# Optimization experiments

Hardware: AMD Instinct MI355X
Metric: run time of the kernel (lower is better)

Reference implementation:

```python
import jax, jax.numpy as jnp
from jax import lax
import numpy as np

N_X, N_Y, N_OBS = 30, 50, 256
ITERS, LR = 400, 0.05


def project_simplex(v):
    # Euclidean projection of a 1-D vector onto the probability simplex.
    n = v.shape[0]
    u = jnp.sort(v)[::-1]
    css = jnp.cumsum(u) - 1.0
    idx = jnp.arange(1, n + 1, dtype=v.dtype)
    rho = jnp.sum((u - css / idx) > 0)
    tau = jnp.take(css, rho - 1) / rho.astype(v.dtype)
    return jnp.maximum(v - tau, 0.0)


def worst_case(r, delta):
    # Exact value of the Ben-Tal et al. total-variation DRO inner problem:
    #   min_{eta, lam>=0} eta + delta*lam + mean_i max(-lam, r_i - eta)
    #   s.t. r_i - eta <= lam
    # = sup_{p in simplex, ||p - 1/N||_1 <= delta} p @ r
    # Closed form: move mass a = min(delta/2, (N-1)/N) from the smallest
    # entries (each holds 1/N nominal mass) onto the largest entry.
    n = r.shape[0]
    nf = jnp.asarray(n, r.dtype)
    a = jnp.minimum(delta * 0.5, (nf - 1.0) / nf)
    s = jnp.sort(r)  # ascending
    w = jnp.clip(a - jnp.arange(n, dtype=r.dtype) / nf, 0.0, 1.0 / nf)
    return jnp.mean(r) + a * jnp.max(r) - jnp.sum(w * s)


def _forward(X, Y, W, b, delta, gamma):
    Y_hat = X @ W.T + b                      # (n_obs, n_y) predictions
    ep = Y - Y_hat                           # (n_obs, n_y) residuals, shared

    def solve_one(y_hat_t):
        # Convex DRO problem per scenario, prisk = p_var: (ep_i @ z - c)^2.
        # Eliminating (eta, lam, obj_aux) analytically via worst_case(), the
        # problem reduces to min over z in simplex, c in R of
        #   worst_case((ep @ z - c)^2, delta) - gamma * (y_hat_t @ z)
        # solved with projected gradient descent (unrolled, fixed iters).
        def obj(z, c):
            r = (ep @ z - c) ** 2            # (n_obs,)
            return worst_case(r, delta) - gamma * jnp.dot(y_hat_t, z)

        z0 = jnp.full((N_Y,), 1.0 / N_Y, dtype=X.dtype)
        c0 = jnp.zeros((), dtype=X.dtype)

        def step(carry, _):
            z, c = carry
            gz, gc = jax.grad(obj, argnums=(0, 1))(z, c)
            return (project_simplex(z - LR * gz), c - LR * gc), None

        (z, _), _ = lax.scan(step, (z0, c0), None, length=ITERS)
        return z

    Z_star = jax.vmap(solve_one)(Y_hat)      # (n_obs, n_y)
    return Z_star, Y_hat


def setup_inputs() -> dict:
    key = jax.random.key(0)
    ks = jax.random.split(key, 6)
    X = jax.random.normal(ks[0], (N_OBS, N_X), dtype=jnp.float32)
    Y = jax.random.normal(ks[1], (N_OBS, N_Y), dtype=jnp.float32)
    # nn.Linear-style init scale
    W = jax.random.normal(ks[2], (N_Y, N_X), dtype=jnp.float32) / np.sqrt(N_X)
    b = jax.random.normal(ks[3], (N_Y,), dtype=jnp.float32) * 0.1
    # torch.rand(1)/5 parameters
    delta = jax.random.uniform(ks[4], (), dtype=jnp.float32) / 5.0
    gamma = jax.random.uniform(ks[5], (), dtype=jnp.float32) / 5.0
    return {"X": X, "Y": Y, "W": W, "b": b, "delta": delta, "gamma": gamma}


def reference(X, Y, W, b, delta, gamma):
    return _forward(X, Y, W, b, delta, gamma)
```

## Files before the change

### kernel.cpp

```cpp
#include <hip/hip_runtime.h>
#include <cfloat>
#include <math.h>

#define NOBS   256
#define NY     50
#define NX     30
#define NITER  400
#define LRATE  0.05f
#define CSTR   260
#define THRANK 40
#define CAND   48

typedef float f32x2 __attribute__((ext_vector_type(2)));

__device__ __forceinline__ float rl_f(float x, int k) {
  return __int_as_float(__builtin_amdgcn_readlane(__float_as_int(x), k));
}
__device__ __forceinline__ int rl_i(int x, int k) {
  return __builtin_amdgcn_readlane(x, k);
}

#define DPP_MAXSTEP(x, ctrl)                                                       \
  x = fmaxf(x, __int_as_float(__builtin_amdgcn_update_dpp(                         \
        __float_as_int(x), __float_as_int(x), (ctrl), 0xF, 0xF, false)))

#define DPP_SUMSTEP(x, ctrl, rmask)                                                \
  x += __int_as_float(__builtin_amdgcn_update_dpp(                                 \
        0, __float_as_int(x), (ctrl), (rmask), 0xF, false))

__device__ __forceinline__ float wave_sum_bcast(float x) {
  DPP_SUMSTEP(x, 0x111, 0xF);
  DPP_SUMSTEP(x, 0x112, 0xF);
  DPP_SUMSTEP(x, 0x114, 0xF);
  DPP_SUMSTEP(x, 0x118, 0xF);
  DPP_SUMSTEP(x, 0x142, 0xA);
  DPP_SUMSTEP(x, 0x143, 0xC);
  return rl_f(x, 63);
}

__global__ __launch_bounds__(512) __attribute__((amdgpu_waves_per_eu(2, 2)))
void dro_kernel(
    const float* __restrict__ X, const float* __restrict__ Y,
    const float* __restrict__ W, const float* __restrict__ Bb,
    const float* __restrict__ DLT, const float* __restrict__ GMM,
    float* __restrict__ out)
{
  __shared__ __align__(16) float smem[51 * CSTR];
  __shared__ __align__(16) unsigned rrk[NOBS];
  __shared__ __align__(16) unsigned ckey[2][128];
  __shared__ __align__(16) float wmax4[4];
  __shared__ __align__(16) int   wtie4[4];
  __shared__ int cctr[2];
  __shared__ unsigned th_key;

  float* const zs  = smem;
  float* const rdx = smem + 512;
  float* const cfs = smem + 1024;

  const int tid  = threadIdx.x;
  const int oid  = tid & 255;
  const int half = tid >> 8;
  const int lane = tid & 63;
  const int w8   = tid >> 6;
  const int wsc  = w8 & 3;
  const int t    = blockIdx.x;

  const float delta = DLT[0];
  const float gamma = GMM[0];
  const float a     = fminf(delta * 0.5f, 255.0f / 256.0f);
  const float a256  = a * 256.0f;

  f32x2 er2[25];
  {
    float xr[NX];
    #pragma unroll
    for (int k = 0; k < NX; ++k) xr[k] = X[oid * NX + k];
    #pragma unroll
    for (int j = 0; j < NY; ++j) {
      float acc = Bb[j];
      #pragma unroll
      for (int k = 0; k < NX; ++k) acc = fmaf(xr[k], W[j * NX + k], acc);
      const float e = Y[oid * NY + j] - acc;
      if (j & 1) er2[j >> 1].y = e; else er2[j >> 1].x = e;
      if (half == 0) smem[j * CSTR + oid] = e;
    }
    if (half == 0) smem[NY * CSTR + oid] = 1.0f;
  }
  float yhl;
  {
    const int jr = (lane < NY) ? lane : 0;
    float acc = Bb[jr];
    #pragma unroll
    for (int k = 0; k < NX; ++k) acc = fmaf(X[t * NX + k], W[jr * NX + k], acc);
    yhl = acc;
    if (tid < NY) out[NOBS * NY + t * NY + tid] = acc;
  }
  if (tid == 0) { th_key = 0xFFFFFFFFu; cctr[0] = 0; cctr[1] = 0; }
  if (tid < CAND) { ckey[0][tid] = 0xFFFFFFFFu; ckey[1][tid] = 0xFFFFFFFFu; }
  __syncthreads();

  f32x2 epb2[16];
  {
    const int colc = (lane < 51) ? lane : 50;
    const float* eb = &smem[colc * CSTR + wsc * 64 + half * 32];
    #pragma unroll
    for (int q = 0; q < 8; ++q) {
      const float4 e4 = *(const float4*)&eb[4 * q];
      epb2[2*q]   = (f32x2){e4.x, e4.y};
      epb2[2*q+1] = (f32x2){e4.z, e4.w};
    }
  }
  __syncthreads();

  float zv = (lane < NY) ? (1.0f / NY) : 0.0f;
  float cc = 0.0f;
  unsigned thk = 0xFFFFFFFFu;
  zs[w8 * 64 + lane] = zv;

  #pragma unroll 1
  for (int it = 0; it < NITER; ++it) {
    const int pp = it & 1;

    const float4* zp = (const float4*)&zs[w8 * 64];
    f32x2 a01 = {0.f, 0.f}, a23 = {0.f, 0.f};
    #pragma unroll
    for (int jq = 0; jq < 12; ++jq) {
      const float4 z4 = zp[jq];
      a01 = __builtin_elementwise_fma(er2[2*jq],   (f32x2){z4.x, z4.y}, a01);
      a23 = __builtin_elementwise_fma(er2[2*jq+1], (f32x2){z4.z, z4.w}, a23);
    }
    {
      const float4 z4 = zp[12];
      a01 = __builtin_elementwise_fma(er2[24], (f32x2){z4.x, z4.y}, a01);
    }
    const float u = ((a01.x + a23.x) + (a01.y + a23.y)) - cc;
    const float r = u * u;
    const unsigned key = __float_as_uint(r);

    float m = r;
    DPP_MAXSTEP(m, 0x111); DPP_MAXSTEP(m, 0x112);
    DPP_MAXSTEP(m, 0x114); DPP_MAXSTEP(m, 0x118);
    DPP_MAXSTEP(m, 0x142); DPP_MAXSTEP(m, 0x143);
    const float mw = rl_f(m, 63);
    const int   wt = __popcll(__ballot(r == mw));

    const bool cond = (key <= thk);
    if (half == 0) {
      rrk[oid] = key;
      const unsigned long long cmask = __ballot(cond);
      const int cpos = __popcll(cmask & ((1ull << lane) - 1ull));
      const int cq   = __popcll(cmask);
      int base = 0;
      if (lane == 0) base = atomicAdd(&cctr[pp], cq);
      base = rl_i(base, 0);
      const int pos = base + cpos;
      if (cond && pos < 128) ckey[pp][pos] = key;
      if (lane == 0) { wmax4[wsc] = mw; wtie4[wsc] = wt; }
    }
    __syncthreads();

    const int Cu = __builtin_amdgcn_readfirstlane(cctr[pp]);
    if (tid == 0) cctr[pp ^ 1] = 0;
    if (tid < CAND) ckey[pp ^ 1][tid] = 0xFFFFFFFFu;

    const float4 wm  = *(const float4*)wmax4;
    const int4   wtv = *(const int4*)wtie4;
    const float mx = fmaxf(fmaxf(wm.x, wm.y), fmaxf(wm.z, wm.w));
    const int   cm = (wm.x == mx ? wtv.x : 0) + (wm.y == mx ? wtv.y : 0)
                   + (wm.z == mx ? wtv.z : 0) + (wm.w == mx ? wtv.w : 0);
    const bool ismax = (r == mx);
    const bool valid = ((float)Cu >= a256) && (Cu <= CAND);

    int cnt;
    if (__builtin_expect(valid, 1)) {
      const uint4* cp = (const uint4*)&ckey[pp][0];
      int n0 = 0, n1 = 0, n2 = 0, n3 = 0;
      #pragma unroll
      for (int jq = 0; jq < CAND / 4; ++jq) {
        const uint4 k4 = cp[jq];
        n0 += (k4.x < key) ? 1 : 0;
        n1 += (k4.y < key) ? 1 : 0;
        n2 += (k4.z < key) ? 1 : 0;
        n3 += (k4.w < key) ? 1 : 0;
      }
      cnt = (n0 + n1) + (n2 + n3);
    } else {
      const uint4* p = (const uint4*)rrk;
      int n0 = 0, n1 = 0, n2 = 0, n3 = 0;
      #pragma unroll 4
      for (int jq = 0; jq < 64; ++jq) {
        const uint4 k4 = p[jq];
        n0 += (k4.x < key) ? 1 : 0;
        n1 += (k4.y < key) ? 1 : 0;
        n2 += (k4.z < key) ? 1 : 0;
        n3 += (k4.w < key) ? 1 : 0;
      }
      cnt = (n0 + n1) + (n2 + n3);
    }
    if (cnt == THRANK && (!valid || cond)) th_key = key;

    const float gfac  = fminf(fmaxf((float)cnt + 1.0f - a256, 0.0f), 1.0f) * (1.0f / 256.0f);
    const float g     = gfac + (ismax ? (a / (float)cm) : 0.0f);
    const float coefv = 2.0f * u * g;

    cfs[w8 * 64 + lane] = coefv;
    const float4* cfp = (const float4*)&cfs[w8 * 64 + half * 32];
    f32x2 qa = {0.f, 0.f}, qb = {0.f, 0.f};
    #pragma unroll
    for (int q = 0; q < 8; ++q) {
      const float4 c4 = cfp[q];
      qa = __builtin_elementwise_fma((f32x2){c4.x, c4.y}, epb2[2*q],   qa);
      qb = __builtin_elementwise_fma((f32x2){c4.z, c4.w}, epb2[2*q+1], qb);
    }
    rdx[w8 * 64 + lane] = (qa.x + qb.x) + (qa.y + qb.y);
    __syncthreads();
    thk = th_key;
    const float r0 = rdx[lane],       r1 = rdx[64 + lane];
    const float r2 = rdx[128 + lane], r3 = rdx[192 + lane];
    const float r4 = rdx[256 + lane], r5 = rdx[320 + lane];
    const float r6 = rdx[384 + lane], r7 = rdx[448 + lane];
    const float s4 = ((r0 + r1) + (r2 + r3)) + ((r4 + r5) + (r6 + r7));
    cc = cc + LRATE * rl_f(s4, NY);
    const float gz = s4 - gamma * yhl;
    const float v  = zv - LRATE * gz;

    float tau = 0.0f;
    {
      bool cur = (lane < NY) && (zv > 0.0f);
      unsigned long long bal = __ballot(cur);
      int   n = __popcll(bal);
      float S = wave_sum_bcast(cur ? v : 0.0f);
      bool done = false;
      #pragma unroll 1
      for (int pass = 0; pass < 8; ++pass) {
        tau = (S - 1.0f) * __builtin_amdgcn_rcpf((float)n);
        const bool nxt = (lane < NY) && (v > tau);
        const unsigned long long nbal = __ballot(nxt);
        if (nbal == bal) { done = true; break; }
        bal = nbal;
        n   = __popcll(nbal);
        S   = wave_sum_bcast(nxt ? v : 0.0f);
      }
      if (__builtin_expect(!done, 0)) {
        bool inm = (lane < NY);
        float Sf = wave_sum_bcast(inm ? v : 0.0f);
        int   nf = NY;
        #pragma unroll 1
        for (int pass = 0; pass < 32; ++pass) {
          tau = (Sf - 1.0f) * __builtin_amdgcn_rcpf((float)nf);
          const bool nin = inm && (v > tau);
          const int  nn  = __popcll(__ballot(nin));
          if (nn == nf) break;
          Sf = wave_sum_bcast(nin ? v : 0.0f);
          nf = nn;
          inm = nin;
        }
      }
    }
    zv = (lane < NY) ? fmaxf(v - tau, 0.0f) : 0.0f;
    zs[w8 * 64 + lane] = zv;
  }

  if (w8 == 0 && lane < NY) out[t * NY + lane] = zv;

}

extern "C" void kernel_launch(void* const* d_in, const int* in_sizes, int n_in,
                              void* d_out, int out_size, void* d_ws, size_t ws_size,
                              hipStream_t stream) {
  (void)in_sizes; (void)n_in; (void)d_ws; (void)ws_size; (void)out_size;
  const float* X   = (const float*)d_in[0];
  const float* Y   = (const float*)d_in[1];
  const float* W   = (const float*)d_in[2];
  const float* B   = (const float*)d_in[3];
  const float* DLT = (const float*)d_in[4];
  const float* GMM = (const float*)d_in[5];
  float* out = (float*)d_out;
  hipLaunchKernelGGL(dro_kernel, dim3(NOBS), dim3(512), 0, stream,
                     X, Y, W, B, DLT, GMM, out);
}
```

Measured before the change: 838.8 us.

## Replace candidate-list rank counting with threshold-key max reduction for sort weights

Instead of gathering candidate keys via atomics into a shared list and counting ranks against it, each wave tracks how many residuals fall at or below the previous iteration's threshold key and the max among them. When exactly k0+1 residuals qualify, the max is the boundary order statistic and the sort weight follows from a comparison. Otherwise it falls back to a full 256-entry rank count and refreshes the threshold key. This drops the atomic, the candidate list and its reset, at the cost of an extra DPP max reduction and a narrower fast path.

```diff
diff --git a/kernel.cpp b/kernel.cpp
--- a/kernel.cpp
+++ b/kernel.cpp
@@ -8,16 +8,11 @@
 #define NITER  400
 #define LRATE  0.05f
 #define CSTR   260
-#define THRANK 40
-#define CAND   48
 
 typedef float f32x2 __attribute__((ext_vector_type(2)));
 
 __device__ __forceinline__ float rl_f(float x, int k) {
   return __int_as_float(__builtin_amdgcn_readlane(__float_as_int(x), k));
-}
-__device__ __forceinline__ int rl_i(int x, int k) {
-  return __builtin_amdgcn_readlane(x, k);
 }
 
 #define DPP_MAXSTEP(x, ctrl)                                                       \
@@ -47,11 +42,8 @@
 {
   __shared__ __align__(16) float smem[51 * CSTR];
   __shared__ __align__(16) unsigned rrk[NOBS];
-  __shared__ __align__(16) unsigned ckey[2][128];
-  __shared__ __align__(16) float wmax4[4];
-  __shared__ __align__(16) int   wtie4[4];
-  __shared__ int cctr[2];
-  __shared__ unsigned th_key;
+  __shared__ __align__(16) float wstat[16];
+  __shared__ unsigned q2_key;
 
   float* const zs  = smem;
   float* const rdx = smem + 512;
@@ -69,6 +61,10 @@
   const float gamma = GMM[0];
   const float a     = fminf(delta * 0.5f, 255.0f / 256.0f);
   const float a256  = a * 256.0f;
+  const float k0f   = floorf(a256);
+  const int   k0i   = (int)k0f;
+  const float R256  = 1.0f / 256.0f;
+  const float frac256 = (k0f + 1.0f - a256) * R256;
 
   f32x2 er2[25];
   {
@@ -95,8 +91,7 @@
     yhl = acc;
     if (tid < NY) out[NOBS * NY + t * NY + tid] = acc;
   }
-  if (tid == 0) { th_key = 0xFFFFFFFFu; cctr[0] = 0; cctr[1] = 0; }
-  if (tid < CAND) { ckey[0][tid] = 0xFFFFFFFFu; ckey[1][tid] = 0xFFFFFFFFu; }
+  if (tid == 0) q2_key = 0xFFFFFFFFu;
   __syncthreads();
 
   f32x2 epb2[16];
@@ -114,13 +109,11 @@
 
   float zv = (lane < NY) ? (1.0f / NY) : 0.0f;
   float cc = 0.0f;
-  unsigned thk = 0xFFFFFFFFu;
+  unsigned q2k = 0xFFFFFFFFu;
   zs[w8 * 64 + lane] = zv;
 
   #pragma unroll 1
   for (int it = 0; it < NITER; ++it) {
-    const int pp = it & 1;
-
     const float4* zp = (const float4*)&zs[w8 * 64];
     f32x2 a01 = {0.f, 0.f}, a23 = {0.f, 0.f};
     #pragma unroll
@@ -144,46 +137,36 @@
     const float mw = rl_f(m, 63);
     const int   wt = __popcll(__ballot(r == mw));
 
-    const bool cond = (key <= thk);
+    const bool condq = (key <= q2k);
+    float mq = condq ? r : -1.0f;
+    DPP_MAXSTEP(mq, 0x111); DPP_MAXSTEP(mq, 0x112);
+    DPP_MAXSTEP(mq, 0x114); DPP_MAXSTEP(mq, 0x118);
+    DPP_MAXSTEP(mq, 0x142); DPP_MAXSTEP(mq, 0x143);
+    const float mqw = rl_f(mq, 63);
+    const int   cq2 = __popcll(__ballot(condq));
+
     if (half == 0) {
       rrk[oid] = key;
-      const unsigned long long cmask = __ballot(cond);
-      const int cpos = __popcll(cmask & ((1ull << lane) - 1ull));
-      const int cq   = __popcll(cmask);
-      int base = 0;
-      if (lane == 0) base = atomicAdd(&cctr[pp], cq);
-      base = rl_i(base, 0);
-      const int pos = base + cpos;
-      if (cond && pos < 128) ckey[pp][pos] = key;
-      if (lane == 0) { wmax4[wsc] = mw; wtie4[wsc] = wt; }
+      if (lane == 0)
+        *(float4*)&wstat[4 * wsc] = make_float4(mw, (float)wt, (float)cq2, mqw);
     }
     __syncthreads();
 
-    const int Cu = __builtin_amdgcn_readfirstlane(cctr[pp]);
-    if (tid == 0) cctr[pp ^ 1] = 0;
-    if (tid < CAND) ckey[pp ^ 1][tid] = 0xFFFFFFFFu;
-
-    const float4 wm  = *(const float4*)wmax4;
-    const int4   wtv = *(const int4*)wtie4;
-    const float mx = fmaxf(fmaxf(wm.x, wm.y), fmaxf(wm.z, wm.w));
-    const int   cm = (wm.x == mx ? wtv.x : 0) + (wm.y == mx ? wtv.y : 0)
-                   + (wm.z == mx ? wtv.z : 0) + (wm.w == mx ? wtv.w : 0);
-    const bool ismax = (r == mx);
-    const bool valid = ((float)Cu >= a256) && (Cu <= CAND);
-
-    int cnt;
-    if (__builtin_expect(valid, 1)) {
-      const uint4* cp = (const uint4*)&ckey[pp][0];
-      int n0 = 0, n1 = 0, n2 = 0, n3 = 0;
-      #pragma unroll
-      for (int jq = 0; jq < CAND / 4; ++jq) {
-        const uint4 k4 = cp[jq];
-        n0 += (k4.x < key) ? 1 : 0;
-        n1 += (k4.y < key) ? 1 : 0;
-        n2 += (k4.z < key) ? 1 : 0;
-        n3 += (k4.w < key) ? 1 : 0;
-      }
-      cnt = (n0 + n1) + (n2 + n3);
+    const float4 s0 = *(const float4*)&wstat[0];
+    const float4 s1 = *(const float4*)&wstat[4];
+    const float4 s2 = *(const float4*)&wstat[8];
+    const float4 s3 = *(const float4*)&wstat[12];
+    const float mx  = fmaxf(fmaxf(s0.x, s1.x), fmaxf(s2.x, s3.x));
+    const float cmf = (s0.x == mx ? s0.y : 0.f) + (s1.x == mx ? s1.y : 0.f)
+                    + (s2.x == mx ? s2.y : 0.f) + (s3.x == mx ? s3.y : 0.f);
+    const float cq2f = (s0.z + s1.z) + (s2.z + s3.z);
+    const float q2r  = fmaxf(fmaxf(s0.w, s1.w), fmaxf(s2.w, s3.w));
+    const bool ismax  = (r == mx);
+    const bool gvalid = (cq2f == k0f + 1.0f);
+
+    float gfac;
+    if (__builtin_expect(gvalid, 1)) {
+      gfac = (r > q2r) ? R256 : ((r == q2r) ? frac256 : 0.0f);
     } else {
       const uint4* p = (const uint4*)rrk;
       int n0 = 0, n1 = 0, n2 = 0, n3 = 0;
@@ -195,12 +178,12 @@
         n2 += (k4.z < key) ? 1 : 0;
         n3 += (k4.w < key) ? 1 : 0;
       }
-      cnt = (n0 + n1) + (n2 + n3);
-    }
-    if (cnt == THRANK && (!valid || cond)) th_key = key;
-
-    const float gfac  = fminf(fmaxf((float)cnt + 1.0f - a256, 0.0f), 1.0f) * (1.0f / 256.0f);
-    const float g     = gfac + (ismax ? (a / (float)cm) : 0.0f);
+      const int cnt = (n0 + n1) + (n2 + n3);
+      gfac = fminf(fmaxf((float)cnt + 1.0f - a256, 0.0f), 1.0f) * R256;
+      if (half == 0 && cnt == k0i) q2_key = key;
+    }
+
+    const float g     = gfac + (ismax ? (a / cmf) : 0.0f);
     const float coefv = 2.0f * u * g;
 
     cfs[w8 * 64 + lane] = coefv;
@@ -214,7 +197,9 @@
     }
     rdx[w8 * 64 + lane] = (qa.x + qb.x) + (qa.y + qb.y);
     __syncthreads();
-    thk = th_key;
+
+    q2k = gvalid ? __float_as_uint(q2r) : q2_key;
+
     const float r0 = rdx[lane],       r1 = rdx[64 + lane];
     const float r2 = rdx[128 + lane], r3 = rdx[192 + lane];
     const float r4 = rdx[256 + lane], r5 = rdx[320 + lane];
```

Result: slower. 1.570 ms (+87.1%).
